# Kernel optimization log

Hardware: AMD Instinct MI355X
Metric: run time of the kernel (lower is better)

The kernel has to match this reference:

```python
import jax, jax.numpy as jnp
import numpy as np

NUM_PROPOSALS = 200000
NUM_OBJECTS = 128
N_CLS = 256
POS_THR = 0.4
NEG_THR = 0.1
REG_FACTOR = 10.0


def _make_boxes(key, n, img=1000.0, max_wh=200.0):
    k1, k2 = jax.random.split(key)
    xy = jax.random.uniform(k1, (n, 2), jnp.float32) * (img - max_wh)
    wh = jax.random.uniform(k2, (n, 2), jnp.float32) * (max_wh - 1.0) + 1.0
    return jnp.concatenate([xy, xy + wh], axis=-1)  # valid xyxy boxes


def setup_inputs() -> dict:
    key = jax.random.key(0)
    k1, k2, k3 = jax.random.split(key, 3)
    return {
        "objectness_score": jax.random.normal(k1, (NUM_PROPOSALS,), jnp.float32),
        "proposals": _make_boxes(k2, NUM_PROPOSALS),
        "gt_bounding_box": _make_boxes(k3, NUM_OBJECTS)[None],  # (1, N, 4)
    }


def _box_iou(b1, b2):
    # b1: (N,4), b2: (M,4) in xyxy -> (N, M)
    a1 = (b1[:, 2] - b1[:, 0]) * (b1[:, 3] - b1[:, 1])
    a2 = (b2[:, 2] - b2[:, 0]) * (b2[:, 3] - b2[:, 1])
    lt = jnp.maximum(b1[:, None, :2], b2[None, :, :2])
    rb = jnp.minimum(b1[:, None, 2:], b2[None, :, 2:])
    wh = jnp.clip(rb - lt, 0.0)
    inter = wh[..., 0] * wh[..., 1]
    return inter / (a1[:, None] + a2[None, :] - inter)


def _rpn_loss(objectness_score, proposals, gt_bounding_box):
    gt = gt_bounding_box[0]                      # (N, 4)
    iou = _box_iou(gt, proposals)                # (N, M)
    N, M = iou.shape
    flat = iou.reshape(-1)                       # (N*M,)

    # top-N best (gt, proposal) pairs, indices only (non-differentiable path)
    _, best_idx = jax.lax.top_k(flat, N)

    key = jax.random.key(42)
    k1, k2, k3 = jax.random.split(key, 3)
    neg_inf = jnp.float32(-jnp.inf)

    # random-priority sampling == randperm + truncate over candidate multiset
    pos_prio = jnp.where(flat > POS_THR, jax.random.uniform(k1, (N * M,)), neg_inf)
    best_prio = jax.random.uniform(k2, (N,))
    cand_prio = jnp.concatenate([best_prio, pos_prio])
    cand_idx = jnp.concatenate([best_idx, jnp.arange(N * M)])

    num_pos = N_CLS // 2   # always filled: best_idx contributes N=128 candidates
    num_neg = N_CLS - num_pos

    sel_p, loc = jax.lax.top_k(cand_prio, num_pos)
    pos_flat = cand_idx[loc]
    pos_valid = jnp.isfinite(sel_p)
    pos_rows = pos_flat // M
    pos_cols = pos_flat % M

    neg_prio = jnp.where(flat < NEG_THR, jax.random.uniform(k3, (N * M,)), neg_inf)
    sel_n, neg_flat = jax.lax.top_k(neg_prio, num_neg)
    neg_valid = jnp.isfinite(sel_n)
    neg_cols = neg_flat % M

    # classification: BCE-with-logits, mean over valid samples
    logits = jnp.concatenate([objectness_score[pos_cols], objectness_score[neg_cols]])
    labels = jnp.concatenate([jnp.ones((num_pos,), jnp.float32), jnp.zeros((num_neg,), jnp.float32)])
    w = jnp.concatenate([pos_valid, neg_valid]).astype(jnp.float32)
    bce = jnp.maximum(logits, 0.0) - logits * labels + jnp.log1p(jnp.exp(-jnp.abs(logits)))
    cls_loss = jnp.sum(bce * w) / jnp.maximum(jnp.sum(w), 1.0)

    d = proposals[pos_cols] - gt[pos_rows]       # (num_pos, 4)
    ad = jnp.abs(d)
    sl1 = jnp.where(ad < 1.0, 0.5 * d * d, ad - 0.5)
    wp = pos_valid.astype(jnp.float32)[:, None]
    reg_loss = jnp.sum(sl1 * wp) / jnp.maximum(jnp.sum(wp) * 4.0, 1.0)

    return cls_loss + REG_FACTOR * reg_loss


def reference(objectness_score, proposals, gt_bounding_box):
    return _rpn_loss(objectness_score, proposals, gt_bounding_box)
```

## Files before the change

kernel.cpp:

```cpp
#include <hip/hip_runtime.h>
#include <stdint.h>

#pragma clang fp contract(off)

typedef unsigned long long u64;
typedef uint32_t u32;

#define M_PROP 200000u
#define N_GT   128u
#define NM     25600000u
#define ASPLIT 2u
#define CSPLIT 4u

#define BCUT 8355840u
#define CCUT 8387584u
#define IB_POS 0x3ECCCCCDu

#define SHARDS 16u
#define SHARD_CAP 4096u
#define ACAP_SHARD 65536u
#define TOPA_CAP 8192u
#define COMP_CAP 8192u
#define ALIST 512u

#define CSLOT(i) counters[(u32)(i) * 64u]

__device__ inline u32 rotl32(u32 x, u32 r) { return __builtin_rotateleft32(x, r); }

__device__ inline u32 lane_prefix(u64 mask) {
  return __builtin_amdgcn_mbcnt_hi((u32)(mask >> 32),
                                   __builtin_amdgcn_mbcnt_lo((u32)mask, 0u));
}

__host__ __device__ inline void tf2x32(u32 k0, u32 k1, u32 x0, u32 x1,
                                       u32& o0, u32& o1) {
  u32 ks0 = k0, ks1 = k1, ks2 = k0 ^ k1 ^ 0x1BD11BDAu;
  x0 += ks0; x1 += ks1;
#ifdef __HIP_DEVICE_COMPILE__
#define TF_R(r) { x0 += x1; x1 = rotl32(x1, r); x1 ^= x0; }
#else
#define TF_R(r) { x0 += x1; x1 = (x1 << r) | (x1 >> (32 - r)); x1 ^= x0; }
#endif
  TF_R(13) TF_R(15) TF_R(26) TF_R(6)
  x0 += ks1; x1 += ks2 + 1u;
  TF_R(17) TF_R(29) TF_R(16) TF_R(24)
  x0 += ks2; x1 += ks0 + 2u;
  TF_R(13) TF_R(15) TF_R(26) TF_R(6)
  x0 += ks0; x1 += ks1 + 3u;
  TF_R(17) TF_R(29) TF_R(16) TF_R(24)
  x0 += ks1; x1 += ks2 + 4u;
  TF_R(13) TF_R(15) TF_R(26) TF_R(6)
  x0 += ks2; x1 += ks0 + 5u;
#undef TF_R
  o0 = x0; o1 = x1;
}

__device__ inline u32 jax_bits32(u32 ka, u32 kb, u32 idx) {
  u32 a, b; tf2x32(ka, kb, 0u, idx, a, b);
  return a ^ b;
}

static void jax_split3(u32& k1a, u32& k1b, u32& k2a, u32& k2b,
                       u32& k3a, u32& k3b) {
  const u32 K0 = 0u, K1 = 42u;
  tf2x32(K0, K1, 0u, 0u, k1a, k1b);
  tf2x32(K0, K1, 0u, 1u, k2a, k2b);
  tf2x32(K0, K1, 0u, 2u, k3a, k3b);
}

__device__ inline u32 wave_append_slot(u32* ctr, bool pred, bool& any) {
  u64 mask = __ballot(pred);
  if (mask == 0ull) { any = false; return 0u; }
  any = true;
  u32 prefix = lane_prefix(mask);
  int leader = __ffsll(mask) - 1;
  u32 base = 0u;
  if ((int)(threadIdx.x & 63u) == leader)
    base = atomicAdd(ctr, (u32)__popcll(mask));
  base = __shfl(base, leader, 64);
  return base + prefix;
}

__device__ inline u32 iouBin(u32 bits) {
  u32 b = (bits - 0x3E800000u) >> 14;
  return b > 1023u ? 1023u : b;
}

__global__ __launch_bounds__(256) void rpn_collect(
    const float4* __restrict__ props, const float4* __restrict__ gt,
    u64* __restrict__ bufA, u64* __restrict__ bufB, u64* __restrict__ bufC,
    u32* __restrict__ counters, u32* __restrict__ gHistA,
    u32 k1a, u32 k1b, u32 k3a, u32 k3b) {
  __shared__ float4 gtS[64];
  __shared__ float gtAreaS[64];
  __shared__ u32 hA[1024];
  __shared__ u32 listA[4][ALIST];
  const u32 tid = threadIdx.x;
  const u32 lane = tid & 63u;
  const u32 wid = tid >> 6;
  const u32 y = blockIdx.y;
  u32 p = blockIdx.x * 256u + tid;
  bool active = p < M_PROP;

  if (y < ASPLIT) {
    const u32 gbase = y * 64u;
    for (u32 i = tid; i < 1024u; i += 256u) hA[i] = 0u;
    for (u32 j = tid; j < 64u; j += 256u) {
      float4 gb = gt[gbase + j];
      gtS[j] = gb;
      gtAreaS[j] = (gb.z - gb.x) * (gb.w - gb.y);
    }
    __syncthreads();
    const u32 shard = (blockIdx.x * ASPLIT + y) & (SHARDS - 1u);
    u32* cntB_g = &CSLOT(16u + shard);
    u32* cntA_g = &CSLOT(32u + shard);
    u64* myBufB = bufB + (size_t)shard * SHARD_CAP;
    u64* myBufA = bufA + (size_t)shard * ACAP_SHARD;

    float4 pb = make_float4(0.f, 0.f, 0.f, 0.f);
    if (active) pb = props[p];
    float pa = (pb.z - pb.x) * (pb.w - pb.y);
    u32 cntA = 0u;

#define PROCESS_A()                                                          \
    {                                                                        \
      for (u32 i = lane; i < cntA; i += 64u) {                               \
        u32 aidx = listA[wid][i];                                            \
        u32 row = aidx / M_PROP;                                             \
        u32 col = aidx - row * M_PROP;                                       \
        float4 pbx = props[col];                                             \
        float4 gbx = gtS[row - gbase];                                       \
        float gax = gtAreaS[row - gbase];                                    \
        float pax = (pbx.z - pbx.x) * (pbx.w - pbx.y);                       \
        float wxx = fminf(gbx.z, pbx.z) - fmaxf(gbx.x, pbx.x);               \
        float wyy = fminf(gbx.w, pbx.w) - fmaxf(gbx.y, pbx.y);               \
        wxx = fmaxf(wxx, 0.0f); wyy = fmaxf(wyy, 0.0f);                      \
        float interx = wxx * wyy;                                            \
        float ioux = interx / (gax + pax - interx);                          \
        u32 ib = __float_as_uint(ioux);                                      \
        bool isA = ioux > 0.25f;                                             \
        if (isA) atomicAdd(&hA[iouBin(ib)], 1u);                             \
        bool anyk;                                                           \
        u32 sk = wave_append_slot(cntA_g, isA, anyk);                        \
        if (isA && sk < ACAP_SHARD)                                          \
          myBufA[sk] = ((u64)ib << 25) | (u64)(0x1FFFFFFu - aidx);           \
        u32 m1 = jax_bits32(k1a, k1b, aidx) >> 9;                            \
        bool keep = isA && (ib > IB_POS) && (m1 >= BCUT);                    \
        bool anyb;                                                           \
        u32 sb2 = wave_append_slot(cntB_g, keep, anyb);                      \
        if (keep && sb2 < SHARD_CAP)                                         \
          myBufB[sb2] = ((u64)m1 << 25) | (u64)(0x1FFFFFFu - (aidx + 128u)); \
      }                                                                      \
      cntA = 0u;                                                             \
    }

    for (u32 gg = 0u; gg < 64u; gg += 4u) {
      bool aa[4];
#pragma unroll
      for (u32 r = 0u; r < 4u; ++r) {
        float4 gb = gtS[gg + r];
        float ga = gtAreaS[gg + r];
        float wx = fminf(gb.z, pb.z) - fmaxf(gb.x, pb.x);
        float wy = fminf(gb.w, pb.w) - fmaxf(gb.y, pb.y);
        wx = fmaxf(wx, 0.0f); wy = fmaxf(wy, 0.0f);
        float inter = wx * wy;
        float uni = ga + pa - inter;
        aa[r] = active && (inter > 0.2499f * uni);
      }
#pragma unroll
      for (u32 r = 0u; r < 4u; ++r) {
        u64 ma = __ballot(aa[r]);
        if (ma) {
          u32 pfx = lane_prefix(ma);
          if (aa[r]) listA[wid][cntA + pfx] = (gbase + gg + r) * M_PROP + p;
          cntA += (u32)__popcll(ma);
        }
      }
      if (cntA > ALIST - 256u) PROCESS_A();
    }
    PROCESS_A();
#undef PROCESS_A

    __syncthreads();
    for (u32 b = tid; b < 1024u; b += 256u) {
      u32 v = hA[b];
      if (v) atomicAdd(&gHistA[b], v);
    }
  } else {
    const u32 gbase = (y - ASPLIT) * 32u;
    for (u32 j = tid; j < 32u; j += 256u) {
      float4 gb = gt[gbase + j];
      gtS[j] = gb;
      gtAreaS[j] = (gb.z - gb.x) * (gb.w - gb.y);
    }
    __syncthreads();
    const u32 shard = (blockIdx.x * CSPLIT + (y - ASPLIT)) & (SHARDS - 1u);
    u32* cntC_g = &CSLOT(shard);
    u64* myBufC = bufC + (size_t)shard * SHARD_CAP;

    u32 idxR = gbase * M_PROP + p;
    for (u32 gg = 0u; gg < 32u; gg += 8u) {
      u32 m3v[8], idxv[8];
      bool pre[8];
#pragma unroll
      for (u32 r = 0u; r < 8u; ++r) {
        idxv[r] = idxR; idxR += M_PROP;
        m3v[r] = jax_bits32(k3a, k3b, idxv[r]) >> 9;
        pre[r] = m3v[r] >= CCUT;
      }
      bool anyp = pre[0] | pre[1] | pre[2] | pre[3] |
                  pre[4] | pre[5] | pre[6] | pre[7];
      u64 mp = __ballot(anyp);
      if (mp) {
        float4 pbx = make_float4(0.f, 0.f, 0.f, 0.f);
        if (active) pbx = props[p];
        float pax = (pbx.z - pbx.x) * (pbx.w - pbx.y);
#pragma unroll
        for (u32 r = 0u; r < 8u; ++r) {
          float4 gb = gtS[gg + r];
          float ga = gtAreaS[gg + r];
          float wx = fminf(gb.z, pbx.z) - fmaxf(gb.x, pbx.x);
          float wy = fminf(gb.w, pbx.w) - fmaxf(gb.y, pbx.y);
          wx = fmaxf(wx, 0.0f); wy = fmaxf(wy, 0.0f);
          float inter = wx * wy;
          float iouX = inter / (ga + pax - inter);
          bool cc = active && pre[r] && (iouX < 0.1f);
          bool any;
          u32 s = wave_append_slot(cntC_g, cc, any);
          if (cc && s < SHARD_CAP)
            myBufC[s] = ((u64)m3v[r] << 25) | (u64)(0x1FFFFFFu - idxv[r]);
        }
      }
    }
  }
}

__global__ __launch_bounds__(256) void rpn_filterA(
    const u64* __restrict__ bufA, const u32* __restrict__ gHistA,
    u32* __restrict__ counters, u64* __restrict__ bufTopA) {
  const u32 tid = threadIdx.x;
  const u32 lane = tid & 63u;
  u32 loc[16]; u32 t = 0u;
  const u32 bbase = lane * 16u;
#pragma unroll
  for (u32 j = 0u; j < 16u; ++j) { loc[j] = gHistA[bbase + j]; t += loc[j]; }
  u32 suf = t;
  for (u32 off = 1u; off < 64u; off <<= 1u) {
    u32 o = __shfl_down(suf, off, 64);
    if (lane + off < 64u) suf += o;
  }
  u32 cum = suf - t;
  u32 cand = 0u; bool found = false;
#pragma unroll
  for (int j = 15; j >= 0; --j) {
    cum += loc[j];
    if (!found && cum >= 128u) { cand = bbase + (u32)j; found = true; }
  }
  for (u32 off = 1u; off < 64u; off <<= 1u) {
    u32 o = __shfl_xor(cand, off, 64);
    cand = o > cand ? o : cand;
  }
  const u32 cut = cand;
  const u32 sh = blockIdx.x & (SHARDS - 1u);
  const u32 chunk = blockIdx.x >> 4;
  u32 n = CSLOT(32u + sh); n = n < ACAP_SHARD ? n : ACAP_SHARD;
  const u64* sb = bufA + (size_t)sh * ACAP_SHARD;
  for (u32 i = chunk * 256u + tid; i < n; i += 16u * 256u) {
    u64 k = sb[i];
    bool keep = iouBin((u32)(k >> 25)) >= cut;
    bool any;
    u32 s = wave_append_slot(&CSLOT(48), keep, any);
    if (keep && s < TOPA_CAP) bufTopA[s] = k;
  }
}

__device__ inline void rank_select(const u64* cand, u32 nc, u64* selKey) {
  const u32 tid = threadIdx.x;
  if (tid < 128u) selKey[tid] = 0ull;
  u64 k[8]; u32 r[8];
#pragma unroll
  for (int j = 0; j < 8; ++j) {
    u32 i = tid + (u32)j * 1024u;
    k[j] = (i < nc) ? cand[i] : 0ull;
    r[j] = 0u;
  }
  __syncthreads();
  for (u32 i = 0u; i < nc; ++i) {
    u64 v = cand[i];
#pragma unroll
    for (int j = 0; j < 8; ++j) r[j] += (v > k[j]) ? 1u : 0u;
  }
#pragma unroll
  for (int j = 0; j < 8; ++j) {
    u32 i = tid + (u32)j * 1024u;
    if (i < nc && r[j] < 128u) selKey[r[j]] = k[j];
  }
  __syncthreads();
}

__device__ inline void rank_select2(const u64* cand, u32 nc, u64* selKey) {
  const u32 tid = threadIdx.x;
  if (tid < 128u) selKey[tid] = 0ull;
  u64 mine = (tid < nc) ? cand[tid] : 0ull;
  __syncthreads();
  u32 r = 0u;
  for (u32 i = 0u; i < nc; ++i) r += (cand[i] > mine) ? 1u : 0u;
  if (tid < nc && r < 128u) selKey[r] = mine;
  __syncthreads();
}

__device__ inline float sl1(float d) {
  float ad = fabsf(d);
  return (ad < 1.0f) ? 0.5f * d * d : ad - 0.5f;
}

__global__ __launch_bounds__(1024) void rpn_finalize(
    const float* __restrict__ obj, const float4* __restrict__ props,
    const float4* __restrict__ gt,
    const u64* __restrict__ bufTopA,
    const u64* __restrict__ bufB, const u64* __restrict__ bufC,
    const u32* __restrict__ counters, float* __restrict__ out,
    u32 k2a, u32 k2b) {
  __shared__ u64 keyBuf[COMP_CAP];
  __shared__ u64 keyBuf2[1024];
  __shared__ u64 selKey[128];
  __shared__ u32 bestIdx[128];
  __shared__ u32 hist64[64];
  __shared__ float pr[16];
  __shared__ u32 s_cnt, s_cnt2, s_cutLo;
  __shared__ float s_reg, s_bcep;

  const u32 tid = threadIdx.x;
  const u32 lane = tid & 63u;
  const u32 wid = tid >> 6u;

  u32 nT = CSLOT(48); nT = nT < TOPA_CAP ? nT : TOPA_CAP;
  for (u32 i = tid; i < nT; i += 1024u) keyBuf[i] = bufTopA[i];
  __syncthreads();
  if (nT <= 1024u) rank_select2(keyBuf, nT, selKey);
  else rank_select(keyBuf, nT, selKey);
  if (tid < 128u) {
    u64 k = selKey[tid];
    bestIdx[tid] = (k == 0ull) ? 0u : (0x1FFFFFFu - (u32)(k & 0x1FFFFFFu));
  }
  __syncthreads();

  if (tid == 0u) { s_cnt = 128u; s_cnt2 = 0u; }
  if (tid < 64u) hist64[tid] = 0u;
  __syncthreads();
  if (tid < 128u) {
    u32 m2 = jax_bits32(k2a, k2b, tid) >> 9;
    keyBuf[tid] = ((u64)m2 << 25) | (u64)(0x1FFFFFFu - tid);
    if (m2 >= BCUT) atomicAdd(&hist64[(m2 - BCUT) >> 9], 1u);
  }
  {
    u32 n = CSLOT(16u + wid); n = n < SHARD_CAP ? n : SHARD_CAP;
    const u64* sb = bufB + (size_t)wid * SHARD_CAP;
    for (u32 i = lane; i < n; i += 64u) {
      u64 k = sb[i];
      bool any;
      u32 s = wave_append_slot(&s_cnt, true, any);
      if (s < COMP_CAP) keyBuf[s] = k;
      atomicAdd(&hist64[((u32)(k >> 25) - BCUT) >> 9], 1u);
    }
  }
  __syncthreads();
  u32 nc = s_cnt < COMP_CAP ? s_cnt : COMP_CAP;
  if (wid == 0u) {
    u32 suf = hist64[lane];
    for (u32 off = 1u; off < 64u; off <<= 1u) {
      u32 o = __shfl_down(suf, off, 64);
      if (lane + off < 64u) suf += o;
    }
    u64 ok = __ballot(suf >= 128u);
    u32 cutLo = 0u;
    if (ok) cutLo = BCUT + ((63u - (u32)__clzll(ok)) << 9);
    if (lane == 0u) s_cutLo = cutLo;
  }
  __syncthreads();
  {
    u64 cutKey = ((u64)s_cutLo) << 25;
    for (u32 i = tid; i < nc; i += 1024u) {
      u64 k = keyBuf[i];
      if (k >= cutKey) {
        u32 s = atomicAdd(&s_cnt2, 1u);
        if (s < 1024u) keyBuf2[s] = k;
      }
    }
  }
  __syncthreads();
  u32 ns = s_cnt2;
  if (ns <= 1024u) rank_select2(keyBuf2, ns, selKey);
  else rank_select(keyBuf, nc, selKey);

  float locReg = 0.0f, locBce = 0.0f;
  if (tid < 128u) {
    u64 k = selKey[tid];
    if (k != 0ull) {
      u32 c = 0x1FFFFFFu - (u32)(k & 0x1FFFFFFu);
      u32 pair = (c < 128u) ? bestIdx[c] : (c - 128u);
      if (pair < NM) {
        u32 row = pair / M_PROP, col = pair % M_PROP;
        float4 prb = props[col];
        float4 gb = gt[row];
        locReg = sl1(prb.x - gb.x) + sl1(prb.y - gb.y) +
                 sl1(prb.z - gb.z) + sl1(prb.w - gb.w);
        float l = obj[col];
        locBce = fmaxf(l, 0.0f) - l + log1pf(expf(-fabsf(l)));
      }
    }
  }
  {
    float v = locReg;
    for (u32 off = 32u; off > 0u; off >>= 1u) v += __shfl_xor(v, off, 64);
    if (lane == 0u) pr[wid] = v;
    __syncthreads();
    if (tid == 0u) {
      float s = 0.0f;
#pragma unroll
      for (u32 w = 0u; w < 16u; ++w) s += pr[w];
      s_reg = s;
    }
    __syncthreads();
    v = locBce;
    for (u32 off = 32u; off > 0u; off >>= 1u) v += __shfl_xor(v, off, 64);
    if (lane == 0u) pr[wid] = v;
    __syncthreads();
    if (tid == 0u) {
      float s = 0.0f;
#pragma unroll
      for (u32 w = 0u; w < 16u; ++w) s += pr[w];
      s_bcep = s;
    }
    __syncthreads();
  }

  if (tid == 0u) { s_cnt = 0u; s_cnt2 = 0u; }
  if (tid < 64u) hist64[tid] = 0u;
  __syncthreads();
  {
    u32 n = CSLOT(wid); n = n < SHARD_CAP ? n : SHARD_CAP;
    const u64* sb = bufC + (size_t)wid * SHARD_CAP;
    for (u32 i = lane; i < n; i += 64u) {
      u64 k = sb[i];
      bool any;
      u32 s = wave_append_slot(&s_cnt, true, any);
      if (s < COMP_CAP) keyBuf[s] = k;
      atomicAdd(&hist64[((u32)(k >> 25) - CCUT) >> 4], 1u);
    }
  }
  __syncthreads();
  nc = s_cnt < COMP_CAP ? s_cnt : COMP_CAP;
  if (wid == 0u) {
    u32 suf = hist64[lane];
    for (u32 off = 1u; off < 64u; off <<= 1u) {
      u32 o = __shfl_down(suf, off, 64);
      if (lane + off < 64u) suf += o;
    }
    u64 ok = __ballot(suf >= 128u);
    u32 cutLo = 0u;
    if (ok) cutLo = CCUT + ((63u - (u32)__clzll(ok)) << 4);
    if (lane == 0u) s_cutLo = cutLo;
  }
  __syncthreads();
  {
    u64 cutKey = ((u64)s_cutLo) << 25;
    for (u32 i = tid; i < nc; i += 1024u) {
      u64 k = keyBuf[i];
      if (k >= cutKey) {
        u32 s = atomicAdd(&s_cnt2, 1u);
        if (s < 1024u) keyBuf2[s] = k;
      }
    }
  }
  __syncthreads();
  ns = s_cnt2;
  if (ns <= 1024u) rank_select2(keyBuf2, ns, selKey);
  else rank_select(keyBuf, nc, selKey);

  float locBceN = 0.0f;
  if (tid < 128u) {
    u64 k = selKey[tid];
    if (k != 0ull) {
      u32 idx = 0x1FFFFFFu - (u32)(k & 0x1FFFFFFu);
      u32 col = idx % M_PROP;
      float l = obj[col];
      locBceN = fmaxf(l, 0.0f) + log1pf(expf(-fabsf(l)));
    }
  }
  {
    float v = locBceN;
    for (u32 off = 32u; off > 0u; off >>= 1u) v += __shfl_xor(v, off, 64);
    if (lane == 0u) pr[wid] = v;
    __syncthreads();
    if (tid == 0u) {
      float s = 0.0f;
#pragma unroll
      for (u32 w = 0u; w < 16u; ++w) s += pr[w];
      float cls = (s_bcep + s) / 256.0f;
      float reg = s_reg / 512.0f;
      out[0] = cls + 10.0f * reg;
    }
  }
}

extern "C" void kernel_launch(void* const* d_in, const int* in_sizes, int n_in,
                              void* d_out, int out_size, void* d_ws, size_t ws_size,
                              hipStream_t stream) {
  (void)in_sizes; (void)n_in; (void)out_size; (void)ws_size;
  const float* obj = (const float*)d_in[0];
  const float4* props = (const float4*)d_in[1];
  const float4* gt = (const float4*)d_in[2];
  float* out = (float*)d_out;

  u32 k1a, k1b, k2a, k2b, k3a, k3b;
  jax_split3(k1a, k1b, k2a, k2b, k3a, k3b);

  uint8_t* base = (uint8_t*)d_ws;
  u32* counters = (u32*)base;
  u32* gHistA = (u32*)(base + 16384);
  u64* bufTopA = (u64*)(base + 16384 + 4096);
  u64* bufB = (u64*)(base + 16384 + 4096 + (size_t)TOPA_CAP * 8);
  u64* bufC = bufB + (size_t)SHARDS * SHARD_CAP;
  u64* bufA = bufC + (size_t)SHARDS * SHARD_CAP;

  const u32 gridX = (M_PROP + 255u) / 256u;
  hipMemsetAsync(d_ws, 0, 16384 + 4096, stream);
  rpn_collect<<<dim3(gridX, ASPLIT + CSPLIT), 256, 0, stream>>>(
      props, gt, bufA, bufB, bufC, counters, gHistA, k1a, k1b, k3a, k3b);
  rpn_filterA<<<256, 256, 0, stream>>>(bufA, gHistA, counters, bufTopA);
  rpn_finalize<<<1, 1024, 0, stream>>>(obj, props, gt, bufTopA, bufB, bufC,
                                       counters, out, k2a, k2b);
}
```

Measured before the change: 102.1 us.

## Convert collect kernel to persistent grid-stride blocks over flattened tiles

The 2D grid (782 x 6) of collect blocks is replaced by a persistent grid of 2048 blocks that stride over a flattened tile index covering both the A (IoU-above-threshold) and C (negative-sampling) work. Each block now accumulates its shared-memory histogram across all its tiles and flushes it to the global histogram once at the end, which cuts global atomics and launch/tail overhead. A launch-bounds occupancy hint is added, and the C path's per-element key-bits call is replaced with inline threefry calls. The cost is an extra block-wide barrier per tile and a less even mix of A and C tiles across blocks, which could cause load imbalance.

Measured after the change: 95.64 us (median of 2 runs). -6.4%, faster.

```diff
diff --git a/kernel.cpp b/kernel.cpp
--- a/kernel.cpp
+++ b/kernel.cpp
@@ -9,8 +9,6 @@
 #define M_PROP 200000u
 #define N_GT   128u
 #define NM     25600000u
-#define ASPLIT 2u
-#define CSPLIT 4u
 
 #define BCUT 8355840u
 #define CCUT 8387584u
@@ -22,6 +20,11 @@
 #define TOPA_CAP 8192u
 #define COMP_CAP 8192u
 #define ALIST 512u
+
+#define NBX 782u
+#define NT_A (NBX * 2u)
+#define NT_ALL (NBX * 6u)
+#define PERSIST 2048u
 
 #define CSLOT(i) counters[(u32)(i) * 64u]
 
@@ -86,7 +89,7 @@
   return b > 1023u ? 1023u : b;
 }
 
-__global__ __launch_bounds__(256) void rpn_collect(
+__global__ __launch_bounds__(256, 8) void rpn_collect(
     const float4* __restrict__ props, const float4* __restrict__ gt,
     u64* __restrict__ bufA, u64* __restrict__ bufB, u64* __restrict__ bufC,
     u32* __restrict__ counters, u32* __restrict__ gHistA,
@@ -98,140 +101,150 @@
   const u32 tid = threadIdx.x;
   const u32 lane = tid & 63u;
   const u32 wid = tid >> 6;
-  const u32 y = blockIdx.y;
-  u32 p = blockIdx.x * 256u + tid;
-  bool active = p < M_PROP;
-
-  if (y < ASPLIT) {
-    const u32 gbase = y * 64u;
-    for (u32 i = tid; i < 1024u; i += 256u) hA[i] = 0u;
-    for (u32 j = tid; j < 64u; j += 256u) {
-      float4 gb = gt[gbase + j];
-      gtS[j] = gb;
-      gtAreaS[j] = (gb.z - gb.x) * (gb.w - gb.y);
-    }
+  for (u32 i = tid; i < 1024u; i += 256u) hA[i] = 0u;
+
+  for (u32 t = blockIdx.x; t < NT_ALL; t += PERSIST) {
     __syncthreads();
-    const u32 shard = (blockIdx.x * ASPLIT + y) & (SHARDS - 1u);
-    u32* cntB_g = &CSLOT(16u + shard);
-    u32* cntA_g = &CSLOT(32u + shard);
-    u64* myBufB = bufB + (size_t)shard * SHARD_CAP;
-    u64* myBufA = bufA + (size_t)shard * ACAP_SHARD;
-
-    float4 pb = make_float4(0.f, 0.f, 0.f, 0.f);
-    if (active) pb = props[p];
-    float pa = (pb.z - pb.x) * (pb.w - pb.y);
-    u32 cntA = 0u;
+    const u32 shard = t & (SHARDS - 1u);
+    if (t < NT_A) {
+      const u32 bx = t >> 1;
+      const u32 gbase = (t & 1u) * 64u;
+      for (u32 j = tid; j < 64u; j += 256u) {
+        float4 gb = gt[gbase + j];
+        gtS[j] = gb;
+        gtAreaS[j] = (gb.z - gb.x) * (gb.w - gb.y);
+      }
+      __syncthreads();
+      u32* cntB_g = &CSLOT(16u + shard);
+      u32* cntA_g = &CSLOT(32u + shard);
+      u64* myBufB = bufB + (size_t)shard * SHARD_CAP;
+      u64* myBufA = bufA + (size_t)shard * ACAP_SHARD;
+
+      u32 p = bx * 256u + tid;
+      bool active = p < M_PROP;
+      float4 pb = make_float4(0.f, 0.f, 0.f, 0.f);
+      if (active) pb = props[p];
+      float pa = (pb.z - pb.x) * (pb.w - pb.y);
+      u32 cntA = 0u;
 
 #define PROCESS_A()                                                          \
-    {                                                                        \
-      for (u32 i = lane; i < cntA; i += 64u) {                               \
-        u32 aidx = listA[wid][i];                                            \
-        u32 row = aidx / M_PROP;                                             \
-        u32 col = aidx - row * M_PROP;                                       \
-        float4 pbx = props[col];                                             \
-        float4 gbx = gtS[row - gbase];                                       \
-        float gax = gtAreaS[row - gbase];                                    \
-        float pax = (pbx.z - pbx.x) * (pbx.w - pbx.y);                       \
-        float wxx = fminf(gbx.z, pbx.z) - fmaxf(gbx.x, pbx.x);               \
-        float wyy = fminf(gbx.w, pbx.w) - fmaxf(gbx.y, pbx.y);               \
-        wxx = fmaxf(wxx, 0.0f); wyy = fmaxf(wyy, 0.0f);                      \
-        float interx = wxx * wyy;                                            \
-        float ioux = interx / (gax + pax - interx);                          \
-        u32 ib = __float_as_uint(ioux);                                      \
-        bool isA = ioux > 0.25f;                                             \
-        if (isA) atomicAdd(&hA[iouBin(ib)], 1u);                             \
-        bool anyk;                                                           \
-        u32 sk = wave_append_slot(cntA_g, isA, anyk);                        \
-        if (isA && sk < ACAP_SHARD)                                          \
-          myBufA[sk] = ((u64)ib << 25) | (u64)(0x1FFFFFFu - aidx);           \
-        u32 m1 = jax_bits32(k1a, k1b, aidx) >> 9;                            \
-        bool keep = isA && (ib > IB_POS) && (m1 >= BCUT);                    \
-        bool anyb;                                                           \
-        u32 sb2 = wave_append_slot(cntB_g, keep, anyb);                      \
-        if (keep && sb2 < SHARD_CAP)                                         \
-          myBufB[sb2] = ((u64)m1 << 25) | (u64)(0x1FFFFFFu - (aidx + 128u)); \
-      }                                                                      \
-      cntA = 0u;                                                             \
-    }
-
-    for (u32 gg = 0u; gg < 64u; gg += 4u) {
-      bool aa[4];
-#pragma unroll
-      for (u32 r = 0u; r < 4u; ++r) {
-        float4 gb = gtS[gg + r];
-        float ga = gtAreaS[gg + r];
-        float wx = fminf(gb.z, pb.z) - fmaxf(gb.x, pb.x);
-        float wy = fminf(gb.w, pb.w) - fmaxf(gb.y, pb.y);
-        wx = fmaxf(wx, 0.0f); wy = fmaxf(wy, 0.0f);
-        float inter = wx * wy;
-        float uni = ga + pa - inter;
-        aa[r] = active && (inter > 0.2499f * uni);
-      }
-#pragma unroll
-      for (u32 r = 0u; r < 4u; ++r) {
-        u64 ma = __ballot(aa[r]);
-        if (ma) {
-          u32 pfx = lane_prefix(ma);
-          if (aa[r]) listA[wid][cntA + pfx] = (gbase + gg + r) * M_PROP + p;
-          cntA += (u32)__popcll(ma);
-        }
-      }
-      if (cntA > ALIST - 256u) PROCESS_A();
-    }
-    PROCESS_A();
-#undef PROCESS_A
-
-    __syncthreads();
-    for (u32 b = tid; b < 1024u; b += 256u) {
-      u32 v = hA[b];
-      if (v) atomicAdd(&gHistA[b], v);
-    }
-  } else {
-    const u32 gbase = (y - ASPLIT) * 32u;
-    for (u32 j = tid; j < 32u; j += 256u) {
-      float4 gb = gt[gbase + j];
-      gtS[j] = gb;
-      gtAreaS[j] = (gb.z - gb.x) * (gb.w - gb.y);
-    }
-    __syncthreads();
-    const u32 shard = (blockIdx.x * CSPLIT + (y - ASPLIT)) & (SHARDS - 1u);
-    u32* cntC_g = &CSLOT(shard);
-    u64* myBufC = bufC + (size_t)shard * SHARD_CAP;
-
-    u32 idxR = gbase * M_PROP + p;
-    for (u32 gg = 0u; gg < 32u; gg += 8u) {
-      u32 m3v[8], idxv[8];
-      bool pre[8];
-#pragma unroll
-      for (u32 r = 0u; r < 8u; ++r) {
-        idxv[r] = idxR; idxR += M_PROP;
-        m3v[r] = jax_bits32(k3a, k3b, idxv[r]) >> 9;
-        pre[r] = m3v[r] >= CCUT;
-      }
-      bool anyp = pre[0] | pre[1] | pre[2] | pre[3] |
-                  pre[4] | pre[5] | pre[6] | pre[7];
-      u64 mp = __ballot(anyp);
-      if (mp) {
-        float4 pbx = make_float4(0.f, 0.f, 0.f, 0.f);
-        if (active) pbx = props[p];
-        float pax = (pbx.z - pbx.x) * (pbx.w - pbx.y);
-#pragma unroll
-        for (u32 r = 0u; r < 8u; ++r) {
+      {                                                                      \
+        for (u32 i = lane; i < cntA; i += 64u) {                             \
+          u32 aidx = listA[wid][i];                                          \
+          u32 row = aidx / M_PROP;                                           \
+          u32 col = aidx - row * M_PROP;                                     \
+          float4 pbx = props[col];                                           \
+          float4 gbx = gtS[row - gbase];                                     \
+          float gax = gtAreaS[row - gbase];                                  \
+          float pax = (pbx.z - pbx.x) * (pbx.w - pbx.y);                     \
+          float wxx = fminf(gbx.z, pbx.z) - fmaxf(gbx.x, pbx.x);             \
+          float wyy = fminf(gbx.w, pbx.w) - fmaxf(gbx.y, pbx.y);             \
+          wxx = fmaxf(wxx, 0.0f); wyy = fmaxf(wyy, 0.0f);                    \
+          float interx = wxx * wyy;                                          \
+          float ioux = interx / (gax + pax - interx);                        \
+          u32 ib = __float_as_uint(ioux);                                    \
+          bool isA = ioux > 0.25f;                                           \
+          if (isA) atomicAdd(&hA[iouBin(ib)], 1u);                           \
+          bool anyk;                                                         \
+          u32 sk = wave_append_slot(cntA_g, isA, anyk);                      \
+          if (isA && sk < ACAP_SHARD)                                        \
+            myBufA[sk] = ((u64)ib << 25) | (u64)(0x1FFFFFFu - aidx);         \
+          u32 m1 = jax_bits32(k1a, k1b, aidx) >> 9;                          \
+          bool keep = isA && (ib > IB_POS) && (m1 >= BCUT);                  \
+          bool anyb;                                                         \
+          u32 sb2 = wave_append_slot(cntB_g, keep, anyb);                    \
+          if (keep && sb2 < SHARD_CAP)                                       \
+            myBufB[sb2] = ((u64)m1 << 25) | (u64)(0x1FFFFFFu - (aidx + 128u)); \
+        }                                                                    \
+        cntA = 0u;                                                           \
+      }
+
+      for (u32 gg = 0u; gg < 64u; gg += 4u) {
+        bool aa[4];
+#pragma unroll
+        for (u32 r = 0u; r < 4u; ++r) {
           float4 gb = gtS[gg + r];
           float ga = gtAreaS[gg + r];
-          float wx = fminf(gb.z, pbx.z) - fmaxf(gb.x, pbx.x);
-          float wy = fminf(gb.w, pbx.w) - fmaxf(gb.y, pbx.y);
+          float wx = fminf(gb.z, pb.z) - fmaxf(gb.x, pb.x);
+          float wy = fminf(gb.w, pb.w) - fmaxf(gb.y, pb.y);
           wx = fmaxf(wx, 0.0f); wy = fmaxf(wy, 0.0f);
           float inter = wx * wy;
-          float iouX = inter / (ga + pax - inter);
-          bool cc = active && pre[r] && (iouX < 0.1f);
-          bool any;
-          u32 s = wave_append_slot(cntC_g, cc, any);
-          if (cc && s < SHARD_CAP)
-            myBufC[s] = ((u64)m3v[r] << 25) | (u64)(0x1FFFFFFu - idxv[r]);
+          float uni = ga + pa - inter;
+          aa[r] = active && (inter > 0.2499f * uni);
         }
-      }
-    }
+#pragma unroll
+        for (u32 r = 0u; r < 4u; ++r) {
+          u64 ma = __ballot(aa[r]);
+          if (ma) {
+            u32 pfx = lane_prefix(ma);
+            if (aa[r]) listA[wid][cntA + pfx] = (gbase + gg + r) * M_PROP + p;
+            cntA += (u32)__popcll(ma);
+          }
+        }
+        if (cntA > ALIST - 256u) PROCESS_A();
+      }
+      PROCESS_A();
+#undef PROCESS_A
+    } else {
+      const u32 ct = t - NT_A;
+      const u32 bx = ct >> 2;
+      const u32 gbase = (ct & 3u) * 32u;
+      for (u32 j = tid; j < 32u; j += 256u) {
+        float4 gb = gt[gbase + j];
+        gtS[j] = gb;
+        gtAreaS[j] = (gb.z - gb.x) * (gb.w - gb.y);
+      }
+      __syncthreads();
+      u32* cntC_g = &CSLOT(shard);
+      u64* myBufC = bufC + (size_t)shard * SHARD_CAP;
+
+      u32 p = bx * 256u + tid;
+      bool active = p < M_PROP;
+
+      for (u32 gg = 0u; gg < 32u; gg += 8u) {
+        const u32 ibase = (gbase + gg) * M_PROP + p;
+#define TFCH(R) u32 m3_##R; { u32 a_, b_; \
+        tf2x32(k3a, k3b, 0u, ibase + (R) * M_PROP, a_, b_); \
+        m3_##R = (a_ ^ b_) >> 9; }
+        TFCH(0) TFCH(1) TFCH(2) TFCH(3) TFCH(4) TFCH(5) TFCH(6) TFCH(7)
+#undef TFCH
+        bool pre0 = m3_0 >= CCUT, pre1 = m3_1 >= CCUT;
+        bool pre2 = m3_2 >= CCUT, pre3 = m3_3 >= CCUT;
+        bool pre4 = m3_4 >= CCUT, pre5 = m3_5 >= CCUT;
+        bool pre6 = m3_6 >= CCUT, pre7 = m3_7 >= CCUT;
+        bool anyp = pre0 | pre1 | pre2 | pre3 | pre4 | pre5 | pre6 | pre7;
+        if (__ballot(anyp)) {
+          float4 pbx = make_float4(0.f, 0.f, 0.f, 0.f);
+          if (active) pbx = props[p];
+          float pax = (pbx.z - pbx.x) * (pbx.w - pbx.y);
+#define CRARE(R)                                                             \
+          {                                                                  \
+            float4 gb = gtS[gg + (R)];                                       \
+            float ga = gtAreaS[gg + (R)];                                    \
+            float wx = fminf(gb.z, pbx.z) - fmaxf(gb.x, pbx.x);              \
+            float wy = fminf(gb.w, pbx.w) - fmaxf(gb.y, pbx.y);              \
+            wx = fmaxf(wx, 0.0f); wy = fmaxf(wy, 0.0f);                      \
+            float inter = wx * wy;                                           \
+            float iouX = inter / (ga + pax - inter);                         \
+            bool cc = active && pre##R && (iouX < 0.1f);                     \
+            bool any_;                                                       \
+            u32 s = wave_append_slot(cntC_g, cc, any_);                      \
+            if (cc && s < SHARD_CAP)                                         \
+              myBufC[s] = ((u64)m3_##R << 25) |                              \
+                          (u64)(0x1FFFFFFu - (ibase + (R) * M_PROP));        \
+          }
+          CRARE(0) CRARE(1) CRARE(2) CRARE(3)
+          CRARE(4) CRARE(5) CRARE(6) CRARE(7)
+#undef CRARE
+        }
+      }
+    }
+  }
+
+  __syncthreads();
+  for (u32 b = tid; b < 1024u; b += 256u) {
+    u32 v = hA[b];
+    if (v) atomicAdd(&gHistA[b], v);
   }
 }
 
@@ -524,9 +537,8 @@
   u64* bufC = bufB + (size_t)SHARDS * SHARD_CAP;
   u64* bufA = bufC + (size_t)SHARDS * SHARD_CAP;
 
-  const u32 gridX = (M_PROP + 255u) / 256u;
   hipMemsetAsync(d_ws, 0, 16384 + 4096, stream);
-  rpn_collect<<<dim3(gridX, ASPLIT + CSPLIT), 256, 0, stream>>>(
+  rpn_collect<<<PERSIST, 256, 0, stream>>>(
       props, gt, bufA, bufB, bufC, counters, gHistA, k1a, k1b, k3a, k3b);
   rpn_filterA<<<256, 256, 0, stream>>>(bufA, gHistA, counters, bufTopA);
   rpn_finalize<<<1, 1024, 0, stream>>>(obj, props, gt, bufTopA, bufB, bufC,
```
